# Optimization experiments

Hardware: AMD Instinct MI355X
Metric: run time of the kernel (lower is better)

Reference implementation:

```python
import jax, jax.numpy as jnp
import numpy as np

B, S, D = 2, 1024, 1024
NH = 8
QK = 512   # qk_dim = 0.5 * D
V = 1024   # v_dim = 1.0 * D
DQK = QK // NH   # 64
DHV = V // NH    # 128
CAP = 15.0       # gate_soft_cap
NORM_EPS = 1e-6
DENOM_EPS = 1e-6


def soft_cap(x, cap):
    return cap * jnp.tanh(x / cap)


def setup_inputs() -> dict:
    key = jax.random.key(0)
    ks = jax.random.split(key, 8)
    s = 0.02
    return {
        "x": jax.random.normal(ks[0], (B, S, D), jnp.float32),
        "Wq": jax.random.normal(ks[1], (QK, D), jnp.float32) * s,
        "Wk": jax.random.normal(ks[2], (QK, D), jnp.float32) * s,
        "Wv": jax.random.normal(ks[3], (V, D), jnp.float32) * s,
        "Wog": jax.random.normal(ks[4], (V, D), jnp.float32) * s,
        "Wi": jax.random.normal(ks[5], (NH, D), jnp.float32) * s,
        "bi": jnp.zeros((NH,), jnp.float32),
        "Wf": jax.random.normal(ks[6], (NH, D), jnp.float32) * s,
        "bf": jnp.ones((NH,), jnp.float32),  # positive forget bias
        "gamma": jnp.ones((V,), jnp.float32),
        "Wout": jax.random.normal(ks[7], (D, V), jnp.float32) * s,
    }


def _mlstm_recurrent(q, k, v, i_pre, f_pre):
    # q,k: [B,S,NH,DQK]; v: [B,S,NH,DHV]; i_pre,f_pre: [B,S,NH]
    f_log = jax.nn.log_sigmoid(f_pre)
    q_s = q * (DQK ** -0.5)
    # move time to leading axis for scan
    xs = (jnp.moveaxis(q_s, 1, 0), jnp.moveaxis(k, 1, 0), jnp.moveaxis(v, 1, 0),
          jnp.moveaxis(i_pre, 1, 0), jnp.moveaxis(f_log, 1, 0))
    C0 = jnp.zeros((B, NH, DQK, DHV), q.dtype)
    n0 = jnp.zeros((B, NH, DQK), q.dtype)
    m0 = jnp.zeros((B, NH), q.dtype)

    def step(carry, xt):
        C, n, m = carry
        qt, kt, vt, it, ft = xt  # [B,NH,*]
        m_new = jnp.maximum(ft + m, it)                      # [B,NH]
        f_act = jnp.exp(ft + m - m_new)
        i_act = jnp.exp(it - m_new)
        C = f_act[..., None, None] * C + i_act[..., None, None] * (kt[..., :, None] * vt[..., None, :])
        n = f_act[..., None] * n + i_act[..., None] * kt
        h_num = jnp.einsum('bhd,bhdv->bhv', qt, C)
        qn = jnp.einsum('bhd,bhd->bh', qt, n)
        denom = jnp.maximum(jnp.abs(qn), jnp.exp(-m_new)) + DENOM_EPS
        h = h_num / denom[..., None]
        return (C, n, m_new), h

    (C, n, m), hs = jax.lax.scan(step, (C0, n0, m0), xs)
    return jnp.moveaxis(hs, 0, 1), (C, n, m)  # h: [B,S,NH,DHV]


def reference(x, Wq, Wk, Wv, Wog, Wi, bi, Wf, bf, gamma, Wout):
    q = (x @ Wq.T).reshape(B, S, NH, DQK)
    k = (x @ Wk.T).reshape(B, S, NH, DQK)
    v = (x @ Wv.T).reshape(B, S, NH, DHV)
    o_pre = x @ Wog.T                                  # [B,S,V]
    i_pre = soft_cap(x @ Wi.T + bi, CAP)               # [B,S,NH]
    f_pre = soft_cap(x @ Wf.T + bf, CAP)               # [B,S,NH]

    h, _state = _mlstm_recurrent(q, k, v, i_pre, f_pre)  # [B,S,NH,DHV]

    # multi-head layernorm over head dim, float32 reductions
    h32 = h.astype(jnp.float32)
    mu = jnp.mean(h32, axis=-1, keepdims=True)
    var = jnp.mean(jnp.square(h32 - mu), axis=-1, keepdims=True)
    h_norm = ((h32 - mu) * jax.lax.rsqrt(var + NORM_EPS)).astype(h.dtype)
    h_norm = h_norm * gamma.reshape(NH, DHV)
    h_norm = h_norm.reshape(B, S, V)

    h_out = jax.nn.sigmoid(o_pre) * h_norm
    y = h_out @ Wout.T
    return y
```

## Files before the change

### kernel.cpp

```cpp
#include <hip/hip_runtime.h>
#include <hip/hip_bf16.h>
#include <math.h>

typedef __bf16 bf16x8 __attribute__((ext_vector_type(8)));
typedef float f32x4 __attribute__((ext_vector_type(4)));

#define NB 2
#define NS 1024
#define ND 1024
#define NH 8
#define NQK 512
#define NV 1024
#define DQK 64
#define DHV 128
#define CHUNK 64
#define NCHUNK 16

#define GLDS16(g, l) __builtin_amdgcn_global_load_lds((const __attribute__((address_space(1))) void*)(g), (__attribute__((address_space(3))) void*)(l), 16, 0, 0)

static __device__ __forceinline__ void split_bf16(float v, __bf16& hi, __bf16& lo) {
  hi = (__bf16)v;
  lo = (__bf16)(v - (float)hi);
}

static __device__ __forceinline__ int xcd_swz(int orig, int nwg) {
  int q = nwg >> 3, r = nwg & 7;
  int xcd = orig & 7, idx = orig >> 3;
  int base = (xcd < r) ? xcd * (q + 1) : r * (q + 1) + (xcd - r) * q;
  return base + idx;
}

__global__ __launch_bounds__(256) void cvt_all(const float* __restrict__ x,
    const float* __restrict__ wq, const float* __restrict__ wk,
    const float* __restrict__ wv, const float* __restrict__ wog,
    const float* __restrict__ wout,
    __bf16* __restrict__ xb, __bf16* __restrict__ wb, __bf16* __restrict__ wob) {
  long i = (long)blockIdx.x * 256 + threadIdx.x;
  const float* src; __bf16* dst;
  if (i < 524288)        { src = x    + i*4;                    dst = xb  + i*4; }
  else if (i < 655360)   { long j = i -  524288; src = wq  + j*4; dst = wb + j*4; }
  else if (i < 786432)   { long j = i -  655360; src = wk  + j*4; dst = wb +  524288 + j*4; }
  else if (i < 1048576)  { long j = i -  786432; src = wv  + j*4; dst = wb + 1048576 + j*4; }
  else if (i < 1310720)  { long j = i - 1048576; src = wog + j*4; dst = wb + 2097152 + j*4; }
  else                   { long j = i - 1310720; src = wout+ j*4; dst = wob + j*4; }
  float4 v = *(const float4*)src;
  __bf16 o[4];
  o[0] = (__bf16)v.x; o[1] = (__bf16)v.y; o[2] = (__bf16)v.z; o[3] = (__bf16)v.w;
  *(short4*)dst = *(const short4*)o;
}

#define GEMM_STAGE(Abuf, Bbuf, Aptr, Bptr, Krun, ktv)                         \
  do {                                                                        \
    _Pragma("unroll")                                                         \
    for (int i_ = 0; i_ < 4; ++i_) {                                          \
      const int sb_ = i_ * 256 + wid * 64;                                    \
      const int s_ = sb_ + lane;                                              \
      const int row_ = s_ >> 3;                                               \
      const int klog_ = (s_ & 7) ^ (row_ & 7);                                \
      GLDS16(Aptr + (size_t)(m0 + row_) * Krun + (ktv) * 64 + klog_ * 8, Abuf + sb_ * 8); \
      GLDS16(Bptr + (size_t)(n0 + row_) * Krun + (ktv) * 64 + klog_ * 8, Bbuf + sb_ * 8); \
    }                                                                         \
  } while (0)

__global__ __launch_bounds__(256) void gemm_bt(const __bf16* __restrict__ A,
                                               const __bf16* __restrict__ Bm,
                                               float* __restrict__ C,
                                               int M, int N, int K, int ntn, int nwg) {
  __shared__ __bf16 smA[2][128 * 64];
  __shared__ __bf16 smB[2][128 * 64];
  const int wg = xcd_swz(blockIdx.x, nwg);
  const int m0 = (wg / ntn) * 128;
  const int n0 = (wg % ntn) * 128;
  const int tid = threadIdx.x;
  const int wid = tid >> 6, lane = tid & 63;
  const int wm = (wid >> 1) * 64, wn = (wid & 1) * 64;
  const int fr = lane & 15;
  const int g  = lane >> 4;
  f32x4 acc[4][4] = {};
  const int NT = K >> 6;
  GEMM_STAGE(smA[0], smB[0], A, Bm, K, 0);
  int cur = 0;
  for (int kt = 0; kt < NT; ++kt) {
    __syncthreads();
    if (kt + 1 < NT) GEMM_STAGE(smA[cur ^ 1], smB[cur ^ 1], A, Bm, K, kt + 1);
    #pragma unroll
    for (int kk = 0; kk < 2; ++kk) {
      const int kg = kk * 4 + g;
      bf16x8 af[4], bfv[4];
      #pragma unroll
      for (int f = 0; f < 4; ++f) {
        const int Ra = wm + f * 16 + fr;
        const int Rb = wn + f * 16 + fr;
        af[f]  = *(const bf16x8*)&smA[cur][Ra * 64 + ((kg ^ (Ra & 7)) * 8)];
        bfv[f] = *(const bf16x8*)&smB[cur][Rb * 64 + ((kg ^ (Rb & 7)) * 8)];
      }
      #pragma unroll
      for (int i = 0; i < 4; ++i)
        #pragma unroll
        for (int j = 0; j < 4; ++j)
          acc[i][j] = __builtin_amdgcn_mfma_f32_16x16x32_bf16(af[i], bfv[j], acc[i][j], 0, 0, 0);
    }
    cur ^= 1;
  }
  const int orow = m0 + wm + g * 4;
  const int ocol = n0 + wn + fr;
  #pragma unroll
  for (int i = 0; i < 4; ++i)
    #pragma unroll
    for (int j = 0; j < 4; ++j)
      #pragma unroll
      for (int r = 0; r < 4; ++r)
        C[(size_t)(orow + i*16 + r) * N + (ocol + j*16)] = acc[i][j][r];
}

__global__ __launch_bounds__(256) void gemm_proj(const __bf16* __restrict__ A,
    const __bf16* __restrict__ Bm,
    __bf16* __restrict__ qh, __bf16* __restrict__ ql,
    __bf16* __restrict__ kh, __bf16* __restrict__ kl,
    __bf16* __restrict__ kT, __bf16* __restrict__ vT,
    _Float16* __restrict__ ogs) {
  __shared__ __bf16 smA[2][128 * 64];
  __shared__ __bf16 smB[2][128 * 64];
  const int wg = xcd_swz(blockIdx.x, 384);
  const int m0 = (wg / 24) * 128;
  const int n0 = (wg % 24) * 128;
  const int tid = threadIdx.x;
  const int wid = tid >> 6, lane = tid & 63;
  const int wm = (wid >> 1) * 64, wn = (wid & 1) * 64;
  const int fr = lane & 15;
  const int g  = lane >> 4;
  f32x4 acc[4][4] = {};
  GEMM_STAGE(smA[0], smB[0], A, Bm, 1024, 0);
  int cur = 0;
  for (int kt = 0; kt < 16; ++kt) {
    __syncthreads();
    if (kt + 1 < 16) GEMM_STAGE(smA[cur ^ 1], smB[cur ^ 1], A, Bm, 1024, kt + 1);
    #pragma unroll
    for (int kk = 0; kk < 2; ++kk) {
      const int kg = kk * 4 + g;
      bf16x8 af[4], bfv[4];
      #pragma unroll
      for (int f = 0; f < 4; ++f) {
        const int Ra = wm + f * 16 + fr;
        const int Rb = wn + f * 16 + fr;
        af[f]  = *(const bf16x8*)&smA[cur][Ra * 64 + ((kg ^ (Ra & 7)) * 8)];
        bfv[f] = *(const bf16x8*)&smB[cur][Rb * 64 + ((kg ^ (Rb & 7)) * 8)];
      }
      #pragma unroll
      for (int i = 0; i < 4; ++i)
        #pragma unroll
        for (int j = 0; j < 4; ++j)
          acc[i][j] = __builtin_amdgcn_mfma_f32_16x16x32_bf16(af[i], bfv[j], acc[i][j], 0, 0, 0);
    }
    cur ^= 1;
  }
  const int orow = m0 + wm + g * 4;
  const int ocol = n0 + wn + fr;
  const int rng = n0 >> 9;
  if (rng == 0 || rng == 1) {
    __bf16* Hb = (rng == 0) ? qh : kh;
    __bf16* Lb = (rng == 0) ? ql : kl;
    const float sc = (rng == 0) ? 0.125f : 1.0f;
    #pragma unroll
    for (int i = 0; i < 4; ++i)
      #pragma unroll
      for (int j = 0; j < 4; ++j) {
        const int col = (ocol + j*16) & 511;
        const int d = col & 63;
        const int hb = col & ~63;
        __bf16 t4[4];
        #pragma unroll
        for (int r = 0; r < 4; ++r) {
          const int row = orow + i*16 + r;
          float v = acc[i][j][r] * sc;
          __bf16 hi, lo; split_bf16(v, hi, lo);
          t4[r] = hi;
          const int off = row*512 + hb + ((((d>>3) ^ (row&7))) << 3) + (d & 7);
          Hb[off] = hi;
          Lb[off] = lo;
        }
        if (rng == 1) {
          const int row0r = orow + i*16;
          const int bh = ((row0r >> 10) << 3) + (col >> 6);
          const int c = (row0r >> 6) & 15;
          const int s0 = (row0r & 63);
          const int off = ((bh*16 + c)*64 + d)*64 + (((s0>>3) ^ (d&7)) << 3) + (s0 & 7);
          *(short4*)&kT[off] = *(const short4*)t4;
        }
      }
  } else if (rng == 2 || rng == 3) {
    #pragma unroll
    for (int i = 0; i < 4; ++i)
      #pragma unroll
      for (int j = 0; j < 4; ++j) {
        const int col = (ocol + j*16) & 1023;
        const int u = col & 127;
        __bf16 t4[4];
        #pragma unroll
        for (int r = 0; r < 4; ++r) t4[r] = (__bf16)acc[i][j][r];
        const int row0r = orow + i*16;
        const int bh = ((row0r >> 10) << 3) + (col >> 7);
        const int c = (row0r >> 6) & 15;
        const int s0 = (row0r & 63);
        const int off = ((bh*16 + c)*128 + u)*64 + (((s0>>3) ^ (u&7)) << 3) + (s0 & 7);
        *(short4*)&vT[off] = *(const short4*)t4;
      }
  } else {
    #pragma unroll
    for (int i = 0; i < 4; ++i)
      #pragma unroll
      for (int j = 0; j < 4; ++j) {
        const int col = (ocol + j*16) & 1023;
        #pragma unroll
        for (int r = 0; r < 4; ++r) {
          const int row = orow + i*16 + r;
          float sg = 1.f / (1.f + __expf(-acc[i][j][r]));
          ogs[(size_t)row*1024 + col] = (_Float16)sg;
        }
      }
  }
}

__global__ __launch_bounds__(256) void ifgate_kernel(const float* __restrict__ x,
    const float* __restrict__ Wi, const float* __restrict__ bi,
    const float* __restrict__ Wf, const float* __restrict__ bf_,
    float* __restrict__ icap, float* __restrict__ flog) {
  const int row = blockIdx.x;
  const int w = threadIdx.x >> 6;
  const int l = threadIdx.x & 63;
  const float* xr = x + (size_t)row * ND;
  float xv[16];
  #pragma unroll
  for (int t = 0; t < 16; ++t) xv[t] = xr[l + 64*t];
  for (int hh = 0; hh < 2; ++hh) {
    int h = w*2 + hh;
    const float* wi = Wi + (size_t)h * ND;
    const float* wf = Wf + (size_t)h * ND;
    float si = 0.f, sf = 0.f;
    #pragma unroll
    for (int t = 0; t < 16; ++t) {
      si += xv[t] * wi[l + 64*t];
      sf += xv[t] * wf[l + 64*t];
    }
    #pragma unroll
    for (int off = 32; off; off >>= 1) {
      si += __shfl_xor(si, off, 64);
      sf += __shfl_xor(sf, off, 64);
    }
    if (l == 0) {
      float ic = 15.f * tanhf((si + bi[h]) * (1.f/15.f));
      float fc = 15.f * tanhf((sf + bf_[h]) * (1.f/15.f));
      float fl = (fc >= 0.f) ? -log1pf(__expf(-fc)) : (fc - log1pf(__expf(fc)));
      icap[row*NH + h] = ic;
      flog[row*NH + h] = fl;
    }
  }
}

__global__ __launch_bounds__(64) void gates_kernel(const float* __restrict__ icap,
    const float* __restrict__ flog, float* __restrict__ g_g, float* __restrict__ a_g,
    float* __restrict__ m_g, float* __restrict__ m0g) {
  const int bh = blockIdx.x;
  const int b = bh >> 3, h = bh & 7;
  const int l = threadIdx.x;
  float m0 = 0.f;
  for (int c = 0; c < NCHUNK; ++c) {
    const int t = c*CHUNK + l;
    const int row = b*NS + t;
    float B = flog[row*NH + h];
    float iv = icap[row*NH + h];
    #pragma unroll
    for (int d = 1; d < 64; d <<= 1) {
      float o = __shfl_up(B, d, 64);
      if (l >= d) B += o;
    }
    float g = iv - B;
    float cm = g;
    #pragma unroll
    for (int d = 1; d < 64; d <<= 1) {
      float o = __shfl_up(cm, d, 64);
      if (l >= d) cm = fmaxf(cm, o);
    }
    float a = fmaxf(m0, cm);
    float m = B + a;
    const int idx = bh*NS + t;
    g_g[idx] = g; a_g[idx] = a; m_g[idx] = m;
    if (l == 0) m0g[bh*NCHUNK + c] = m0;
    m0 = __shfl(m, 63, 64);
  }
}

__global__ __launch_bounds__(256) void u_kernel(const __bf16* __restrict__ kT,
    const __bf16* __restrict__ vT, const float* __restrict__ g_g,
    const float* __restrict__ a_g, float* __restrict__ Ut, float* __restrict__ Ung) {
  __shared__ __bf16 kts[64 * 64];
  __shared__ __bf16 vts[128 * 64];
  __shared__ float w_l[64];
  const int task = blockIdx.x;
  const int bh = task >> 4, c = task & 15;
  const int t = threadIdx.x;
  const int wid = t >> 6, lane = t & 63;
  const int fr = lane & 15, g = lane >> 4;
  if (t < 64) {
    const float aL = a_g[bh*NS + c*CHUNK + 63];
    w_l[t] = __expf(g_g[bh*NS + c*CHUNK + t] - aL);
  }
  {
    const int sb = wid * 64;
    #pragma unroll
    for (int i = 0; i < 2; ++i) {
      const int s = i*256 + sb + lane;
      GLDS16(kT + (size_t)task*4096 + s*8, kts + (i*256 + sb)*8);
    }
    #pragma unroll
    for (int i = 0; i < 4; ++i) {
      const int s = i*256 + sb + lane;
      GLDS16(vT + (size_t)task*8192 + s*8, vts + (i*256 + sb)*8);
    }
  }
  __syncthreads();
  f32x4 acc[8] = {};
  #pragma unroll
  for (int kk = 0; kk < 2; ++kk) {
    const int kg = kk*4 + g;
    const int Ra = wid*16 + fr;
    bf16x8 afr = *(const bf16x8*)&kts[Ra*64 + ((kg ^ (Ra & 7)) * 8)];
    bf16x8 afw;
    #pragma unroll
    for (int j = 0; j < 8; ++j) afw[j] = (__bf16)((float)afr[j] * w_l[kg*8 + j]);
    #pragma unroll
    for (int nt = 0; nt < 8; ++nt) {
      const int Rb = nt*16 + fr;
      bf16x8 bv = *(const bf16x8*)&vts[Rb*64 + ((kg ^ (Rb & 7)) * 8)];
      acc[nt] = __builtin_amdgcn_mfma_f32_16x16x32_bf16(afw, bv, acc[nt], 0, 0, 0);
    }
  }
  float* ub = Ut + (size_t)task * 8192;
  #pragma unroll
  for (int nt = 0; nt < 8; ++nt) {
    const int u = nt*16 + fr;
    *(f32x4*)&ub[u*64 + wid*16 + g*4] = acc[nt];
  }
  if (t < 64) {
    float s = 0.f;
    #pragma unroll
    for (int blk = 0; blk < 8; ++blk) {
      bf16x8 kv = *(const bf16x8*)&kts[t*64 + ((blk ^ (t & 7)) * 8)];
      #pragma unroll
      for (int j = 0; j < 8; ++j) s += (float)kv[j] * w_l[blk*8 + j];
    }
    Ung[task*64 + t] = s;
  }
}

__global__ __launch_bounds__(512) void statescan_kernel(const float* __restrict__ Ut,
    const float* __restrict__ Ung, const float* __restrict__ m0g,
    const float* __restrict__ a_g, __bf16* __restrict__ C0T, float* __restrict__ n0g) {
  const int bh = blockIdx.x >> 1, part = blockIdx.x & 1;
  const int e8 = part*512 + threadIdx.x;
  const int u = e8 >> 3, d8 = e8 & 7;
  const int dsto = u*64 + ((d8 ^ (u & 7)) << 3);
  const int srco = u*64 + d8*8;
  float scale[NCHUNK];
  #pragma unroll
  for (int c = 0; c < NCHUNK; ++c)
    scale[c] = __expf(m0g[bh*NCHUNK + c] - a_g[bh*NS + c*CHUNK + 63]);
  float val[8] = {};
  for (int c = 0; c < NCHUNK; ++c) {
    const size_t base = ((size_t)(bh*NCHUNK + c)) * 8192;
    __bf16 o[8];
    #pragma unroll
    for (int j = 0; j < 8; ++j) o[j] = (__bf16)val[j];
    *(float4*)&C0T[base + dsto] = *(const float4*)o;
    f32x4 u0 = *(const f32x4*)&Ut[base + srco];
    f32x4 u1 = *(const f32x4*)&Ut[base + srco + 4];
    #pragma unroll
    for (int j = 0; j < 4; ++j) {
      val[j]   = scale[c]*val[j]   + u0[j];
      val[j+4] = scale[c]*val[j+4] + u1[j];
    }
  }
  if (part == 0 && threadIdx.x < 64) {
    float nv = 0.f;
    for (int c = 0; c < NCHUNK; ++c) {
      int idx = (bh*NCHUNK + c)*64 + threadIdx.x;
      n0g[idx] = nv;
      nv = scale[c]*nv + Ung[idx];
    }
  }
}

__global__ __launch_bounds__(256) void intra_kernel(
    const __bf16* __restrict__ qh, const __bf16* __restrict__ ql,
    const __bf16* __restrict__ kh, const __bf16* __restrict__ kl,
    const __bf16* __restrict__ vT, const __bf16* __restrict__ C0T,
    const _Float16* __restrict__ ogs,
    const float* __restrict__ g_g, const float* __restrict__ a_g,
    const float* __restrict__ m_g, const float* __restrict__ m0g,
    const float* __restrict__ n0g,
    const float* __restrict__ gamma, __bf16* __restrict__ hout) {
  __shared__ __bf16 qh_s[32*64], ql_s[32*64];
  __shared__ __bf16 kh_s[64*64], kl_s[64*64];
  __shared__ __bf16 vt_s[128*64];
  __shared__ __bf16 c0_s[128*64];
  __shared__ __bf16 Ps[32*72];
  __shared__ float g_l[64], n0_l[64], a_l[32], m_l[32], cI_l[32];
  __shared__ float qnA[2][32], qnI_l[32], lnS[2][32], lnQ[2][32];

  const int blk = blockIdx.x;
  const int task = blk >> 1, jhalf = blk & 1;
  const int bh = task >> 4, c = task & 15;
  const int b = bh >> 3, h = bh & 7;
  const int t = threadIdx.x;
  const int wid = t >> 6, lane = t & 63;
  const int fr = lane & 15, lg = lane >> 4;
  const int jt_local = wid >> 1, half = wid & 1;
  const int jtg = jhalf*2 + jt_local;
  const int row0 = b*NS + c*CHUNK;
  const int jrow0 = row0 + jhalf*32;

  {
    const int sb = wid * 64;
    {
      const int s = sb + lane;
      const int r = s >> 3, bk = s & 7;
      const size_t go = (size_t)(jrow0 + r)*512 + h*64 + bk*8;
      GLDS16(qh + go, qh_s + sb*8);
      GLDS16(ql + go, ql_s + sb*8);
    }
    #pragma unroll
    for (int i = 0; i < 2; ++i) {
      const int s = i*256 + sb + lane;
      const int r = s >> 3, bk = s & 7;
      const size_t go = (size_t)(row0 + r)*512 + h*64 + bk*8;
      GLDS16(kh + go, kh_s + (i*256 + sb)*8);
      GLDS16(kl + go, kl_s + (i*256 + sb)*8);
    }
    #pragma unroll
    for (int i = 0; i < 4; ++i) {
      const int s = i*256 + sb + lane;
      GLDS16(vT  + (size_t)task*8192 + s*8, vt_s + (i*256 + sb)*8);
      GLDS16(C0T + (size_t)task*8192 + s*8, c0_s + (i*256 + sb)*8);
    }
  }
  const float m0v = m0g[bh*NCHUNK + c];
  if (t < 64) {
    g_l[t]  = g_g[bh*NS + c*CHUNK + t];
    n0_l[t] = n0g[task*64 + t];
  } else if (t < 96) {
    int jl = t - 64;
    float av = a_g[bh*NS + c*CHUNK + jhalf*32 + jl];
    a_l[jl] = av;
    m_l[jl] = m_g[bh*NS + c*CHUNK + jhalf*32 + jl];
    cI_l[jl] = __expf(m0v - av);
  }
  __syncthreads();

  float rsum[4] = {0.f, 0.f, 0.f, 0.f};
  for (int st = half; st < 4; st += 2) {
    if (st <= jtg) {
      f32x4 sacc = {};
      #pragma unroll
      for (int kk = 0; kk < 2; ++kk) {
        const int kg = kk*4 + lg;
        const int Ra = jt_local*16 + fr;
        const int Rb = st*16 + fr;
        bf16x8 qhv = *(const bf16x8*)&qh_s[Ra*64 + ((kg ^ (Ra&7))*8)];
        bf16x8 qlv = *(const bf16x8*)&ql_s[Ra*64 + ((kg ^ (Ra&7))*8)];
        bf16x8 khv = *(const bf16x8*)&kh_s[Rb*64 + ((kg ^ (Rb&7))*8)];
        bf16x8 klv = *(const bf16x8*)&kl_s[Rb*64 + ((kg ^ (Rb&7))*8)];
        sacc = __builtin_amdgcn_mfma_f32_16x16x32_bf16(qhv, khv, sacc, 0, 0, 0);
        sacc = __builtin_amdgcn_mfma_f32_16x16x32_bf16(qhv, klv, sacc, 0, 0, 0);
        sacc = __builtin_amdgcn_mfma_f32_16x16x32_bf16(qlv, khv, sacc, 0, 0, 0);
      }
      const int s_c = st*16 + fr;
      const float gs = g_l[s_c];
      #pragma unroll
      for (int r = 0; r < 4; ++r) {
        const int jl = jt_local*16 + lg*4 + r;
        const int j_c = jhalf*32 + jl;
        float w = (s_c <= j_c) ? __expf(gs - a_l[jl]) : 0.f;
        float p = sacc[r] * w;
        rsum[r] += p;
        Ps[jl*72 + s_c] = (__bf16)p;
      }
    } else {
      #pragma unroll
      for (int r = 0; r < 4; ++r)
        Ps[(jt_local*16 + lg*4 + r)*72 + st*16 + fr] = (__bf16)0.f;
    }
  }
  #pragma unroll
  for (int r = 0; r < 4; ++r) {
    #pragma unroll
    for (int off = 1; off < 16; off <<= 1) rsum[r] += __shfl_xor(rsum[r], off, 64);
  }
  if (fr == 0) {
    #pragma unroll
    for (int r = 0; r < 4; ++r) qnA[half][jt_local*16 + lg*4 + r] = rsum[r];
  }

  f32x4 acc[4] = {};
  #pragma unroll
  for (int kk = 0; kk < 2; ++kk) {
    const int kg = kk*4 + lg;
    const int Ra = jt_local*16 + fr;
    bf16x8 aq = *(const bf16x8*)&qh_s[Ra*64 + ((kg ^ (Ra&7))*8)];
    #pragma unroll
    for (int nt = 0; nt < 4; ++nt) {
      const int Rb = (half*4 + nt)*16 + fr;
      bf16x8 bc = *(const bf16x8*)&c0_s[Rb*64 + ((kg ^ (Rb&7))*8)];
      acc[nt] = __builtin_amdgcn_mfma_f32_16x16x32_bf16(aq, bc, acc[nt], 0, 0, 0);
    }
  }
  {
    float ci4[4];
    #pragma unroll
    for (int r = 0; r < 4; ++r) ci4[r] = cI_l[jt_local*16 + lg*4 + r];
    #pragma unroll
    for (int nt = 0; nt < 4; ++nt)
      #pragma unroll
      for (int r = 0; r < 4; ++r) acc[nt][r] *= ci4[r];
  }
  if (half == 1) {
    const int jl = jt_local*16 + fr;
    float s = 0.f;
    #pragma unroll
    for (int i = 0; i < 16; ++i) {
      const int d = lg*16 + i;
      const int off = jl*64 + (((d>>3) ^ (jl&7)) << 3) + (d & 7);
      float qv = (float)qh_s[off] + (float)ql_s[off];
      s += qv * n0_l[d];
    }
    s += __shfl_xor(s, 16, 64);
    s += __shfl_xor(s, 32, 64);
    if (lane < 16) qnI_l[jl] = cI_l[jl] * s;
  }
  __syncthreads();

  #pragma unroll
  for (int kk = 0; kk < 2; ++kk) {
    const int kg = kk*4 + lg;
    bf16x8 ap = *(const bf16x8*)&Ps[(jt_local*16 + fr)*72 + kg*8];
    #pragma unroll
    for (int nt = 0; nt < 4; ++nt) {
      const int Rb = (half*4 + nt)*16 + fr;
      bf16x8 bv = *(const bf16x8*)&vt_s[Rb*64 + ((kg ^ (Rb&7))*8)];
      acc[nt] = __builtin_amdgcn_mfma_f32_16x16x32_bf16(ap, bv, acc[nt], 0, 0, 0);
    }
  }

  #pragma unroll
  for (int r = 0; r < 4; ++r) {
    const int jl = jt_local*16 + lg*4 + r;
    float qn = qnA[0][jl] + qnA[1][jl] + qnI_l[jl];
    float denom = fmaxf(fabsf(qn), __expf(-m_l[jl])) + 1e-6f;
    float rd = 1.f / denom;
    float s = 0.f, q2 = 0.f;
    #pragma unroll
    for (int nt = 0; nt < 4; ++nt) {
      float hv = acc[nt][r] * rd;
      acc[nt][r] = hv;
      s += hv; q2 += hv*hv;
    }
    #pragma unroll
    for (int off = 1; off < 16; off <<= 1) {
      s  += __shfl_xor(s,  off, 64);
      q2 += __shfl_xor(q2, off, 64);
    }
    if (fr == 0) { lnS[half][jl] = s; lnQ[half][jl] = q2; }
  }
  __syncthreads();

  #pragma unroll
  for (int r = 0; r < 4; ++r) {
    const int jl = jt_local*16 + lg*4 + r;
    float sm = lnS[0][jl] + lnS[1][jl];
    float sq = lnQ[0][jl] + lnQ[1][jl];
    float mu = sm * (1.f/128.f);
    float var = sq * (1.f/128.f) - mu*mu;
    float rstd = rsqrtf(var + 1e-6f);
    const int rowg = jrow0 + jl;
    #pragma unroll
    for (int nt = 0; nt < 4; ++nt) {
      const int u = (half*4 + nt)*16 + fr;
      float sg = (float)ogs[(size_t)rowg*1024 + h*DHV + u];
      float hn = (acc[nt][r] - mu) * rstd * gamma[h*DHV + u] * sg;
      hout[(size_t)rowg*NV + h*DHV + u] = (__bf16)hn;
    }
  }
}

extern "C" void kernel_launch(void* const* d_in, const int* in_sizes, int n_in,
                              void* d_out, int out_size, void* d_ws, size_t ws_size,
                              hipStream_t stream) {
  const float* x    = (const float*)d_in[0];
  const float* Wq   = (const float*)d_in[1];
  const float* Wk   = (const float*)d_in[2];
  const float* Wv   = (const float*)d_in[3];
  const float* Wog  = (const float*)d_in[4];
  const float* Wi   = (const float*)d_in[5];
  const float* bi   = (const float*)d_in[6];
  const float* Wf   = (const float*)d_in[7];
  const float* bf_  = (const float*)d_in[8];
  const float* gamma= (const float*)d_in[9];
  const float* Wout = (const float*)d_in[10];
  float* y = (float*)d_out;

  char* ws = (char*)d_ws;
  const size_t MB = 1u << 20;
  __bf16*   xb   = (__bf16*)  (ws + 0);
  __bf16*   Wb   = (__bf16*)  (ws + 4*MB);
  __bf16*   Wob  = (__bf16*)  (ws + 10*MB);
  __bf16*   qh   = (__bf16*)  (ws + 12*MB);
  __bf16*   ql   = (__bf16*)  (ws + 14*MB);
  __bf16*   kh   = (__bf16*)  (ws + 16*MB);
  __bf16*   kl   = (__bf16*)  (ws + 18*MB);
  __bf16*   kT   = (__bf16*)  (ws + 20*MB);
  __bf16*   vT   = (__bf16*)  (ws + 22*MB);
  _Float16* ogs  = (_Float16*)(ws + 26*MB);
  float*    Ut   = (float*)   (ws + 30*MB);
  __bf16*   C0T  = (__bf16*)  (ws + 38*MB);
  float*    icap = (float*)   (ws + 42*MB);
  float*    flog = (float*)   (ws + 42*MB + 64*1024);
  float*    g_g  = (float*)   (ws + 42*MB + 128*1024);
  float*    a_g  = (float*)   (ws + 42*MB + 192*1024);
  float*    m_g  = (float*)   (ws + 42*MB + 256*1024);
  float*    m0g  = (float*)   (ws + 42*MB + 320*1024);
  float*    Ung  = (float*)   (ws + 42*MB + 384*1024);
  float*    n0g  = (float*)   (ws + 42*MB + 448*1024);
  __bf16*   houtb= (__bf16*)  (ws + 44*MB);

  cvt_all<<<6144, 256, 0, stream>>>(x, Wq, Wk, Wv, Wog, Wout, xb, Wb, Wob);

  gemm_proj<<<384, 256, 0, stream>>>(xb, Wb, qh, ql, kh, kl, kT, vT, ogs);

  ifgate_kernel<<<2048, 256, 0, stream>>>(x, Wi, bi, Wf, bf_, icap, flog);
  gates_kernel<<<16, 64, 0, stream>>>(icap, flog, g_g, a_g, m_g, m0g);
  u_kernel<<<256, 256, 0, stream>>>(kT, vT, g_g, a_g, Ut, Ung);
  statescan_kernel<<<32, 512, 0, stream>>>(Ut, Ung, m0g, a_g, C0T, n0g);
  intra_kernel<<<512, 256, 0, stream>>>(qh, ql, kh, kl, vT, C0T, ogs,
                                        g_g, a_g, m_g, m0g, n0g, gamma, houtb);

  gemm_bt<<<128, 256, 0, stream>>>(houtb, Wob, y, 2048, 1024, 1024, 8, 128);
}
```

Baseline: 176.4 us.

## Stage projection epilogue through LDS for coalesced stores; split statescan into more blocks

The gemm_proj epilogue for the q/k hi-lo outputs and the sigmoid output-gate now writes packed values into a swizzled LDS bounce buffer and then emits 16-byte row-contiguous global stores. Previously these were scattered 2-byte stores, which waste memory transactions. The statescan kernel is relaunched as 256 blocks of 64 threads instead of 32 blocks of 512, spreading the serial chunk scan over more CUs. The cost is extra LDS traffic and two more barriers in the epilogue, and there are fewer threads per block in the scan.

New measurement: 183.3 us. 3.9% more time.

```diff
diff --git a/kernel.cpp b/kernel.cpp
--- a/kernel.cpp
+++ b/kernel.cpp
@@ -21,6 +21,12 @@
 static __device__ __forceinline__ void split_bf16(float v, __bf16& hi, __bf16& lo) {
   hi = (__bf16)v;
   lo = (__bf16)(v - (float)hi);
+}
+static __device__ __forceinline__ unsigned short bf2u(__bf16 v) {
+  union { __bf16 b; unsigned short u; } c; c.b = v; return c.u;
+}
+static __device__ __forceinline__ unsigned short hf2u(_Float16 v) {
+  union { _Float16 h; unsigned short u; } c; c.h = v; return c.u;
 }
 
 static __device__ __forceinline__ int xcd_swz(int orig, int nwg) {
@@ -119,8 +125,9 @@
     __bf16* __restrict__ kh, __bf16* __restrict__ kl,
     __bf16* __restrict__ kT, __bf16* __restrict__ vT,
     _Float16* __restrict__ ogs) {
-  __shared__ __bf16 smA[2][128 * 64];
-  __shared__ __bf16 smB[2][128 * 64];
+  __shared__ __align__(16) char smbuf[65536];
+  __bf16* const smAb = (__bf16*)smbuf;
+  __bf16* const smBb = (__bf16*)(smbuf + 32768);
   const int wg = xcd_swz(blockIdx.x, 384);
   const int m0 = (wg / 24) * 128;
   const int n0 = (wg % 24) * 128;
@@ -130,11 +137,11 @@
   const int fr = lane & 15;
   const int g  = lane >> 4;
   f32x4 acc[4][4] = {};
-  GEMM_STAGE(smA[0], smB[0], A, Bm, 1024, 0);
+  GEMM_STAGE(smAb, smBb, A, Bm, 1024, 0);
   int cur = 0;
   for (int kt = 0; kt < 16; ++kt) {
     __syncthreads();
-    if (kt + 1 < 16) GEMM_STAGE(smA[cur ^ 1], smB[cur ^ 1], A, Bm, 1024, kt + 1);
+    if (kt + 1 < 16) GEMM_STAGE(smAb + (cur^1)*8192, smBb + (cur^1)*8192, A, Bm, 1024, kt + 1);
     #pragma unroll
     for (int kk = 0; kk < 2; ++kk) {
       const int kg = kk * 4 + g;
@@ -143,8 +150,8 @@
       for (int f = 0; f < 4; ++f) {
         const int Ra = wm + f * 16 + fr;
         const int Rb = wn + f * 16 + fr;
-        af[f]  = *(const bf16x8*)&smA[cur][Ra * 64 + ((kg ^ (Ra & 7)) * 8)];
-        bfv[f] = *(const bf16x8*)&smB[cur][Rb * 64 + ((kg ^ (Rb & 7)) * 8)];
+        af[f]  = *(const bf16x8*)&smAb[cur*8192 + Ra * 64 + ((kg ^ (Ra & 7)) * 8)];
+        bfv[f] = *(const bf16x8*)&smBb[cur*8192 + Rb * 64 + ((kg ^ (Rb & 7)) * 8)];
       }
       #pragma unroll
       for (int i = 0; i < 4; ++i)
@@ -157,38 +164,7 @@
   const int orow = m0 + wm + g * 4;
   const int ocol = n0 + wn + fr;
   const int rng = n0 >> 9;
-  if (rng == 0 || rng == 1) {
-    __bf16* Hb = (rng == 0) ? qh : kh;
-    __bf16* Lb = (rng == 0) ? ql : kl;
-    const float sc = (rng == 0) ? 0.125f : 1.0f;
-    #pragma unroll
-    for (int i = 0; i < 4; ++i)
-      #pragma unroll
-      for (int j = 0; j < 4; ++j) {
-        const int col = (ocol + j*16) & 511;
-        const int d = col & 63;
-        const int hb = col & ~63;
-        __bf16 t4[4];
-        #pragma unroll
-        for (int r = 0; r < 4; ++r) {
-          const int row = orow + i*16 + r;
-          float v = acc[i][j][r] * sc;
-          __bf16 hi, lo; split_bf16(v, hi, lo);
-          t4[r] = hi;
-          const int off = row*512 + hb + ((((d>>3) ^ (row&7))) << 3) + (d & 7);
-          Hb[off] = hi;
-          Lb[off] = lo;
-        }
-        if (rng == 1) {
-          const int row0r = orow + i*16;
-          const int bh = ((row0r >> 10) << 3) + (col >> 6);
-          const int c = (row0r >> 6) & 15;
-          const int s0 = (row0r & 63);
-          const int off = ((bh*16 + c)*64 + d)*64 + (((s0>>3) ^ (d&7)) << 3) + (s0 & 7);
-          *(short4*)&kT[off] = *(const short4*)t4;
-        }
-      }
-  } else if (rng == 2 || rng == 3) {
+  if (rng == 2 || rng == 3) {
     #pragma unroll
     for (int i = 0; i < 4; ++i)
       #pragma unroll
@@ -206,18 +182,74 @@
         *(short4*)&vT[off] = *(const short4*)t4;
       }
   } else {
+    if (rng == 1) {
+      #pragma unroll
+      for (int i = 0; i < 4; ++i)
+        #pragma unroll
+        for (int j = 0; j < 4; ++j) {
+          const int col = (ocol + j*16) & 511;
+          const int d = col & 63;
+          __bf16 t4[4];
+          #pragma unroll
+          for (int r = 0; r < 4; ++r) t4[r] = (__bf16)acc[i][j][r];
+          const int row0r = orow + i*16;
+          const int bh = ((row0r >> 10) << 3) + (col >> 6);
+          const int c = (row0r >> 6) & 15;
+          const int s0 = (row0r & 63);
+          const int off = ((bh*16 + c)*64 + d)*64 + (((s0>>3) ^ (d&7)) << 3) + (s0 & 7);
+          *(short4*)&kT[off] = *(const short4*)t4;
+        }
+    }
+    __syncthreads();
+    ushort2* bounce = (ushort2*)smbuf;
+    const float sc = (rng == 0) ? 0.125f : 1.0f;
     #pragma unroll
     for (int i = 0; i < 4; ++i)
       #pragma unroll
-      for (int j = 0; j < 4; ++j) {
-        const int col = (ocol + j*16) & 1023;
+      for (int j = 0; j < 4; ++j)
         #pragma unroll
         for (int r = 0; r < 4; ++r) {
-          const int row = orow + i*16 + r;
-          float sg = 1.f / (1.f + __expf(-acc[i][j][r]));
-          ogs[(size_t)row*1024 + col] = (_Float16)sg;
+          const int lrow = wm + i*16 + g*4 + r;
+          const int lcol = wn + j*16 + fr;
+          ushort2 pk;
+          if (rng < 2) {
+            __bf16 hi, lo; split_bf16(acc[i][j][r] * sc, hi, lo);
+            pk.x = bf2u(hi); pk.y = bf2u(lo);
+          } else {
+            _Float16 sg = (_Float16)(1.f / (1.f + __expf(-acc[i][j][r])));
+            pk.x = hf2u(sg); pk.y = 0;
+          }
+          bounce[lrow*128 + (lcol ^ ((lrow & 7) << 3))] = pk;
         }
+    __syncthreads();
+    const int rrow = tid >> 1;
+    const int rbase = (tid & 1) * 8;
+    const int grow = m0 + rrow;
+    #pragma unroll
+    for (int b8 = 0; b8 < 8; ++b8) {
+      const int cc = rbase + b8;
+      const int a = rrow*128 + ((cc ^ (rrow & 7)) << 3);
+      ushort2 p8[8];
+      *(float4*)&p8[0] = *(const float4*)&bounce[a];
+      *(float4*)&p8[4] = *(const float4*)&bounce[a + 4];
+      unsigned short hi8[8], lo8[8];
+      #pragma unroll
+      for (int z = 0; z < 8; ++z) { hi8[z] = p8[z].x; lo8[z] = p8[z].y; }
+      const int coll = cc * 8;
+      if (rng < 2) {
+        const int colt = (n0 & 511) + coll;
+        const int d8 = (colt & 63) >> 3;
+        const int hb = colt & ~63;
+        __bf16* Hb = (rng == 0) ? qh : kh;
+        __bf16* Lb = (rng == 0) ? ql : kl;
+        const size_t off = (size_t)grow*512 + hb + ((d8 ^ (grow & 7)) << 3);
+        *(float4*)&Hb[off] = *(const float4*)hi8;
+        *(float4*)&Lb[off] = *(const float4*)lo8;
+      } else {
+        const int colt = (n0 & 1023) + coll;
+        *(float4*)&ogs[(size_t)grow*1024 + colt] = *(const float4*)hi8;
       }
+    }
   }
 }
 
@@ -353,11 +385,11 @@
   }
 }
 
-__global__ __launch_bounds__(512) void statescan_kernel(const float* __restrict__ Ut,
+__global__ __launch_bounds__(64) void statescan_kernel(const float* __restrict__ Ut,
     const float* __restrict__ Ung, const float* __restrict__ m0g,
     const float* __restrict__ a_g, __bf16* __restrict__ C0T, float* __restrict__ n0g) {
-  const int bh = blockIdx.x >> 1, part = blockIdx.x & 1;
-  const int e8 = part*512 + threadIdx.x;
+  const int bh = blockIdx.x >> 4, part = blockIdx.x & 15;
+  const int e8 = part*64 + threadIdx.x;
   const int u = e8 >> 3, d8 = e8 & 7;
   const int dsto = u*64 + ((d8 ^ (u & 7)) << 3);
   const int srco = u*64 + d8*8;
@@ -380,7 +412,7 @@
       val[j+4] = scale[c]*val[j+4] + u1[j];
     }
   }
-  if (part == 0 && threadIdx.x < 64) {
+  if (part == 0) {
     float nv = 0.f;
     for (int c = 0; c < NCHUNK; ++c) {
       int idx = (bh*NCHUNK + c)*64 + threadIdx.x;
@@ -638,7 +670,7 @@
   ifgate_kernel<<<2048, 256, 0, stream>>>(x, Wi, bi, Wf, bf_, icap, flog);
   gates_kernel<<<16, 64, 0, stream>>>(icap, flog, g_g, a_g, m_g, m0g);
   u_kernel<<<256, 256, 0, stream>>>(kT, vT, g_g, a_g, Ut, Ung);
-  statescan_kernel<<<32, 512, 0, stream>>>(Ut, Ung, m0g, a_g, C0T, n0g);
+  statescan_kernel<<<256, 64, 0, stream>>>(Ut, Ung, m0g, a_g, C0T, n0g);
   intra_kernel<<<512, 256, 0, stream>>>(qh, ql, kh, kl, vT, C0T, ogs,
                                         g_g, a_g, m_g, m0g, n0g, gamma, houtb);
 
```
